# Kernel tuning notes

Hardware: AMD Instinct MI355X
Metric: run time of the kernel (lower is better)

The kernel has to match this reference:

```python
import jax, jax.numpy as jnp
import numpy as np

TANFOV = 1.0  # tan(FoV/2) for a 90-degree camera (both axes)
C0 = 0.28209479177387814
C1 = 0.4886025119029199
C2 = (1.0925484305920792, -1.0925484305920792, 0.31539156525252005, -1.0925484305920792, 0.5462742152960396)
C3 = (-0.5900435899266435, 2.890611442640554, -0.4570457994644658, 0.3731763325901154, -0.4570457994644658, 1.445305721320277, -0.5900435899266435)


def eval_sh3(sh, d):
    # sh: [N,16,3], d: [N,3] unit view dirs -> clamped RGB [N,3]
    x, y, z = d[:, 0:1], d[:, 1:2], d[:, 2:3]
    xx, yy, zz = x * x, y * y, z * z
    xy, yz, xz = x * y, y * z, x * z
    res = (C0 * sh[:, 0] - C1 * y * sh[:, 1] + C1 * z * sh[:, 2] - C1 * x * sh[:, 3]
           + C2[0] * xy * sh[:, 4] + C2[1] * yz * sh[:, 5] + C2[2] * (2 * zz - xx - yy) * sh[:, 6]
           + C2[3] * xz * sh[:, 7] + C2[4] * (xx - yy) * sh[:, 8]
           + C3[0] * y * (3 * xx - yy) * sh[:, 9] + C3[1] * xy * z * sh[:, 10]
           + C3[2] * y * (4 * zz - xx - yy) * sh[:, 11] + C3[3] * z * (2 * zz - 3 * xx - 3 * yy) * sh[:, 12]
           + C3[4] * x * (4 * zz - xx - yy) * sh[:, 13] + C3[5] * z * (xx - yy) * sh[:, 14]
           + C3[6] * x * (xx - 3 * yy) * sh[:, 15])
    return jnp.maximum(res + 0.5, 0.0)


def quat_to_rot(q):
    w, x, y, z = q[:, 0], q[:, 1], q[:, 2], q[:, 3]
    r0 = jnp.stack([1 - 2 * (y * y + z * z), 2 * (x * y - w * z), 2 * (x * z + w * y)], -1)
    r1 = jnp.stack([2 * (x * y + w * z), 1 - 2 * (x * x + z * z), 2 * (y * z - w * x)], -1)
    r2 = jnp.stack([2 * (x * z - w * y), 2 * (y * z + w * x), 1 - 2 * (x * x + y * y)], -1)
    return jnp.stack([r0, r1, r2], -2)  # [N,3,3]


def gaussian_render(xyz, scaling, rotation, opacity, features_dc, features_rest,
                    viewmatrix, projmatrix, campos, bg, H, W):
    N = xyz.shape[0]
    # --- activation wrappers (GaussianModel properties) ---
    scales = jnp.exp(scaling)                      # [N,3]
    op = jax.nn.sigmoid(opacity)[:, 0]             # [N]
    qn = rotation / jnp.maximum(jnp.linalg.norm(rotation, axis=-1, keepdims=True), 1e-12)
    shs = jnp.concatenate([features_dc, features_rest], axis=1)  # [N,16,3]
    # --- SH -> RGB ---
    dirs = xyz - campos[None, :]
    dirs = dirs / jnp.maximum(jnp.linalg.norm(dirs, axis=-1, keepdims=True), 1e-12)
    colors = eval_sh3(shs, dirs)                   # [N,3]
    # --- 3D covariance: Sigma = R S S^T R^T ---
    R = quat_to_rot(qn)
    M = R * scales[:, None, :]
    Sigma = M @ jnp.swapaxes(M, -1, -2)            # [N,3,3]
    # --- camera space (torch row-vector convention: p_view = p @ V[:3,:3] + V[3,:3]) ---
    t = xyz @ viewmatrix[:3, :3] + viewmatrix[3, :3]
    tz = t[:, 2]
    fx = W / (2.0 * TANFOV)
    fy = H / (2.0 * TANFOV)
    lim = 1.3 * TANFOV
    tz_safe = jnp.where(jnp.abs(tz) > 1e-6, tz, 1e-6)
    txz = jnp.clip(t[:, 0] / tz_safe, -lim, lim) * tz_safe
    tyz = jnp.clip(t[:, 1] / tz_safe, -lim, lim) * tz_safe
    zeros = jnp.zeros_like(tz)
    J = jnp.stack([jnp.stack([fx / tz_safe, zeros, -fx * txz / (tz_safe * tz_safe)], -1),
                   jnp.stack([zeros, fy / tz_safe, -fy * tyz / (tz_safe * tz_safe)], -1)], -2)  # [N,2,3]
    Wr = viewmatrix[:3, :3].T
    Tm = J @ Wr[None, :, :]                        # [N,2,3]
    cov2 = Tm @ Sigma @ jnp.swapaxes(Tm, -1, -2)   # [N,2,2]
    a = cov2[:, 0, 0] + 0.3
    b = cov2[:, 0, 1]
    c = cov2[:, 1, 1] + 0.3
    det = a * c - b * b
    valid = (tz > 0.2) & (det > 0)
    inv_det = 1.0 / jnp.where(det > 0, det, 1.0)
    conA, conB, conC = c * inv_det, -b * inv_det, a * inv_det
    # --- screen radius (3 sigma of max eigenvalue) ---
    mid = 0.5 * (a + c)
    lam = mid + jnp.sqrt(jnp.maximum(mid * mid - det, 0.1))
    radii = jnp.where(valid, jnp.ceil(3.0 * jnp.sqrt(lam)), 0.0)
    # --- project means with full_proj_transform ---
    p_hom = jnp.concatenate([xyz, jnp.ones((N, 1), xyz.dtype)], axis=1) @ projmatrix
    pw = 1.0 / (p_hom[:, 3] + 1e-7)
    mx = ((p_hom[:, 0] * pw + 1.0) * W - 1.0) * 0.5
    my = ((p_hom[:, 1] * pw + 1.0) * H - 1.0) * 0.5
    # --- per-pixel Gaussian evaluation ---
    ys, xs = jnp.meshgrid(jnp.arange(H, dtype=xyz.dtype), jnp.arange(W, dtype=xyz.dtype), indexing='ij')
    px = xs.reshape(-1)  # [HW]
    py = ys.reshape(-1)
    dx = px[:, None] - mx[None, :]                 # [HW,N]
    dy = py[:, None] - my[None, :]
    power = -0.5 * (conA[None, :] * dx * dx + conC[None, :] * dy * dy) - conB[None, :] * dx * dy
    alpha = jnp.minimum(0.99, op[None, :] * jnp.exp(jnp.minimum(power, 0.0)))
    skip = (power > 0) | (alpha < (1.0 / 255.0)) | (~valid)[None, :]
    alpha = jnp.where(skip, 0.0, alpha)
    # --- global depth sort + front-to-back alpha compositing ---
    order = jnp.argsort(tz)
    alpha_s = alpha[:, order]
    cols_s = colors[order]
    tz_s = tz[order]
    Tcum = jnp.cumprod(1.0 - alpha_s, axis=1)      # [HW,N]
    Texcl = jnp.concatenate([jnp.ones((H * W, 1), alpha_s.dtype), Tcum[:, :-1]], axis=1)
    wgt = alpha_s * Texcl                          # [HW,N]
    img = wgt @ cols_s + Tcum[:, -1:] * bg[None, :]
    color = img.reshape(H, W, 3).transpose(2, 0, 1)          # [3,H,W]
    depth = (wgt @ tz_s[:, None]).reshape(1, H, W)           # [1,H,W]
    amap = (1.0 - Tcum[:, -1]).reshape(1, H, W)              # [1,H,W]
    return color, depth, amap, radii


def setup_inputs() -> dict:
    key = jax.random.key(0)
    ks = jax.random.split(key, 6)
    N, H, W = 2048, 128, 128
    xyz = 0.7 * jax.random.normal(ks[0], (N, 3), jnp.float32)
    scaling = jnp.log(0.03) + 0.3 * jax.random.normal(ks[1], (N, 3), jnp.float32)
    rotation = jax.random.normal(ks[2], (N, 4), jnp.float32)
    opacity = jax.random.normal(ks[3], (N, 1), jnp.float32) - 1.0
    features_dc = 0.5 * jax.random.normal(ks[4], (N, 1, 3), jnp.float32)
    features_rest = 0.05 * jax.random.normal(ks[5], (N, 15, 3), jnp.float32)
    # camera at (0,0,-4) looking down +z; transposed (row-vector) matrices as in torch 3DGS
    view = np.eye(4, dtype=np.float32)
    view[3, 2] = 4.0
    znear, zfar = 0.01, 100.0
    P = np.zeros((4, 4), dtype=np.float32)
    P[0, 0] = 1.0 / TANFOV
    P[1, 1] = 1.0 / TANFOV
    P[2, 2] = zfar / (zfar - znear)
    P[3, 2] = -(zfar * znear) / (zfar - znear)
    P[2, 3] = 1.0
    full_proj = view @ P
    campos = jnp.array([0.0, 0.0, -4.0], jnp.float32)
    bg = jnp.zeros(3, jnp.float32)
    return {"xyz": xyz, "scaling": scaling, "rotation": rotation, "opacity": opacity,
            "features_dc": features_dc, "features_rest": features_rest,
            "viewmatrix": jnp.asarray(view), "projmatrix": jnp.asarray(full_proj),
            "campos": campos, "bg": bg, "image_height": H, "image_width": W}


def reference(xyz, scaling, rotation, opacity, features_dc, features_rest,
              viewmatrix, projmatrix, campos, bg, image_height, image_width):
    return gaussian_render(xyz, scaling, rotation, opacity, features_dc, features_rest,
                           viewmatrix, projmatrix, campos, bg, int(image_height), int(image_width))
```

## Files before the change

### kernel.cpp

```cpp
#include <hip/hip_runtime.h>
#include <math.h>

#define TANFOV 1.0f

#define REC   12
#define CHG   256
#define SEG_L 128

__global__ __launch_bounds__(256)
void pre_count_kernel(
    const float* __restrict__ xyz, const float* __restrict__ scaling,
    const float* __restrict__ rotation, const float* __restrict__ opacity,
    const float* __restrict__ fdc, const float* __restrict__ frest,
    const float* __restrict__ vm, const float* __restrict__ pm,
    const float* __restrict__ campos,
    const int* __restrict__ pH, const int* __restrict__ pW,
    float* __restrict__ pre, float4* __restrict__ bboxpre,
    int* __restrict__ rankpart, float* __restrict__ radii_out,
    int N, int NB, int NJ)
{
    __shared__ float s_fr[256 * 45];
    const int tid = threadIdx.x;
    const int bid = blockIdx.x;

    if (bid >= NB) {
        float* s_tz = s_fr;
        int t = bid - NB;
        int col = t / NJ, seg = t - col * NJ;
        int base = seg * SEG_L;
        float c2 = vm[2], c6 = vm[6], c10 = vm[10], c14 = vm[14];
        if (tid < SEG_L) {
            int j = base + tid;
            s_tz[tid] = (j < N)
                ? xyz[j*3+0]*c2 + xyz[j*3+1]*c6 + xyz[j*3+2]*c10 + c14
                : 3.4e38f;
        }
        __syncthreads();

        int i = col * 256 + tid;
        if (i < N) {
            float key = xyz[i*3+0]*c2 + xyz[i*3+1]*c6 + xyz[i*3+2]*c10 + c14;
            int cnt = 0;
            #pragma unroll 8
            for (int j = 0; j < SEG_L; j += 4) {
                float4 v = *reinterpret_cast<float4*>(&s_tz[j]);
                cnt += (v.x < key) || (v.x == key && (base + j)     < i);
                cnt += (v.y < key) || (v.y == key && (base + j + 1) < i);
                cnt += (v.z < key) || (v.z == key && (base + j + 2) < i);
                cnt += (v.w < key) || (v.w == key && (base + j + 3) < i);
            }
            rankpart[seg * N + i] = cnt;
        }
        return;
    }

    int i0 = bid * 256;
    int cnt = N - i0; if (cnt > 256) cnt = 256;
    for (int t = tid; t < cnt * 45; t += 256)
        s_fr[t] = frest[(size_t)i0 * 45 + t];
    __syncthreads();

    int i = i0 + tid;
    if (i >= N) return;
    float H = (float)*pH, W = (float)*pW;

    float px_ = xyz[i*3+0], py_ = xyz[i*3+1], pz_ = xyz[i*3+2];
    float s0 = expf(scaling[i*3+0]), s1 = expf(scaling[i*3+1]), s2 = expf(scaling[i*3+2]);
    float op = 1.f / (1.f + expf(-opacity[i]));

    float qw = rotation[i*4+0], qx = rotation[i*4+1], qy = rotation[i*4+2], qz = rotation[i*4+3];
    float qn = fmaxf(sqrtf(qw*qw + qx*qx + qy*qy + qz*qz), 1e-12f);
    qw /= qn; qx /= qn; qy /= qn; qz /= qn;

    float R00 = 1.f - 2.f*(qy*qy + qz*qz), R01 = 2.f*(qx*qy - qw*qz), R02 = 2.f*(qx*qz + qw*qy);
    float R10 = 2.f*(qx*qy + qw*qz), R11 = 1.f - 2.f*(qx*qx + qz*qz), R12 = 2.f*(qy*qz - qw*qx);
    float R20 = 2.f*(qx*qz - qw*qy), R21 = 2.f*(qy*qz + qw*qx), R22 = 1.f - 2.f*(qx*qx + qy*qy);

    float M00 = R00*s0, M01 = R01*s1, M02 = R02*s2;
    float M10 = R10*s0, M11 = R11*s1, M12 = R12*s2;
    float M20 = R20*s0, M21 = R21*s1, M22 = R22*s2;

    float S00 = M00*M00 + M01*M01 + M02*M02;
    float S01 = M00*M10 + M01*M11 + M02*M12;
    float S02 = M00*M20 + M01*M21 + M02*M22;
    float S11 = M10*M10 + M11*M11 + M12*M12;
    float S12 = M10*M20 + M11*M21 + M12*M22;
    float S22 = M20*M20 + M21*M21 + M22*M22;

    float t0 = px_*vm[0] + py_*vm[4] + pz_*vm[8]  + vm[12];
    float t1 = px_*vm[1] + py_*vm[5] + pz_*vm[9]  + vm[13];
    float tz = px_*vm[2] + py_*vm[6] + pz_*vm[10] + vm[14];

    float fx = W / (2.f * TANFOV), fy = H / (2.f * TANFOV);
    float lim = 1.3f * TANFOV;
    float tzs = (fabsf(tz) > 1e-6f) ? tz : 1e-6f;
    float txz = fminf(fmaxf(t0 / tzs, -lim), lim) * tzs;
    float tyz = fminf(fmaxf(t1 / tzs, -lim), lim) * tzs;
    float J00 = fx / tzs, J02 = -fx * txz / (tzs * tzs);
    float J11 = fy / tzs, J12 = -fy * tyz / (tzs * tzs);

    float T00 = J00*vm[0] + J02*vm[2];
    float T01 = J00*vm[4] + J02*vm[6];
    float T02 = J00*vm[8] + J02*vm[10];
    float T10 = J11*vm[1] + J12*vm[2];
    float T11 = J11*vm[5] + J12*vm[6];
    float T12 = J11*vm[9] + J12*vm[10];

    float u0 = S00*T00 + S01*T01 + S02*T02;
    float u1 = S01*T00 + S11*T01 + S12*T02;
    float u2 = S02*T00 + S12*T01 + S22*T02;
    float v0 = S00*T10 + S01*T11 + S02*T12;
    float v1 = S01*T10 + S11*T11 + S12*T12;
    float v2 = S02*T10 + S12*T11 + S22*T12;
    float a  = T00*u0 + T01*u1 + T02*u2 + 0.3f;
    float b  = T10*u0 + T11*u1 + T12*u2;
    float c  = T10*v0 + T11*v1 + T12*v2 + 0.3f;

    float det = a*c - b*b;
    bool valid = (tz > 0.2f) && (det > 0.f);
    float inv_det = 1.f / ((det > 0.f) ? det : 1.f);
    float conA = c * inv_det, conB = -b * inv_det, conC = a * inv_det;
    float mid = 0.5f * (a + c);
    float lam = mid + sqrtf(fmaxf(mid*mid - det, 0.1f));
    radii_out[i] = valid ? ceilf(3.f * sqrtf(lam)) : 0.f;

    float h0 = px_*pm[0] + py_*pm[4] + pz_*pm[8]  + pm[12];
    float h1 = px_*pm[1] + py_*pm[5] + pz_*pm[9]  + pm[13];
    float h3 = px_*pm[3] + py_*pm[7] + pz_*pm[11] + pm[15];
    float pw = 1.f / (h3 + 1e-7f);
    float mx = ((h0*pw + 1.f) * W - 1.f) * 0.5f;
    float my = ((h1*pw + 1.f) * H - 1.f) * 0.5f;

    float ddx = px_ - campos[0], ddy = py_ - campos[1], ddz = pz_ - campos[2];
    float dn = fmaxf(sqrtf(ddx*ddx + ddy*ddy + ddz*ddz), 1e-12f);
    float x = ddx/dn, y = ddy/dn, z = ddz/dn;
    float xx = x*x, yy = y*y, zz = z*z, xy = x*y, yz = y*z, xz = x*z;

    float basis[16];
    basis[0]  = 0.28209479177387814f;
    basis[1]  = -0.4886025119029199f * y;
    basis[2]  =  0.4886025119029199f * z;
    basis[3]  = -0.4886025119029199f * x;
    basis[4]  =  1.0925484305920792f * xy;
    basis[5]  = -1.0925484305920792f * yz;
    basis[6]  =  0.31539156525252005f * (2.f*zz - xx - yy);
    basis[7]  = -1.0925484305920792f * xz;
    basis[8]  =  0.5462742152960396f * (xx - yy);
    basis[9]  = -0.5900435899266435f * y * (3.f*xx - yy);
    basis[10] =  2.890611442640554f  * xy * z;
    basis[11] = -0.4570457994644658f * y * (4.f*zz - xx - yy);
    basis[12] =  0.3731763325901154f * z * (2.f*zz - 3.f*xx - 3.f*yy);
    basis[13] = -0.4570457994644658f * x * (4.f*zz - xx - yy);
    basis[14] =  1.445305721320277f  * z * (xx - yy);
    basis[15] = -0.5900435899266435f * x * (xx - 3.f*yy);

    const float* fr = &s_fr[tid * 45];
    float col[3];
    #pragma unroll
    for (int ch = 0; ch < 3; ++ch) {
        float r = basis[0] * fdc[i*3 + ch];
        #pragma unroll
        for (int j = 1; j < 16; ++j)
            r += basis[j] * fr[(j-1)*3 + ch];
        col[ch] = fmaxf(r + 0.5f, 0.f);
    }

    float opv = valid ? op : 0.f;
    float4* rec = (float4*)(pre + (size_t)i * REC);
    rec[0] = make_float4(tz, -0.5f*conA, -conB, -0.5f*conC);
    rec[1] = make_float4(mx, my, opv, 0.f);
    rec[2] = make_float4(col[0], col[1], col[2], 0.f);

    float4 bb;
    if (opv > 1.f/255.f) {
        float Rr = 1.01f * sqrtf(2.f * logf(255.f * opv) * lam) + 1.f;
        bb = make_float4(mx - Rr, mx + Rr, my - Rr, my + Rr);
    } else {
        bb = make_float4(1e30f, -1e30f, 1e30f, -1e30f);
    }
    bboxpre[i] = bb;
}

__global__ void scatter_kernel(const int* __restrict__ rankpart,
                               int* __restrict__ perm, int N, int NJ)
{
    int i = blockIdx.x * blockDim.x + threadIdx.x;
    if (i >= N) return;
    int rank = 0;
    for (int s = 0; s < NJ; ++s) rank += rankpart[s * N + i];
    perm[rank] = i;
}

__global__ void blend1_kernel(const float4* __restrict__ grec,
                              const float4* __restrict__ bbox,
                              const int* __restrict__ perm,
                              const int* __restrict__ pW,
                              float* __restrict__ part,
                              int N, int HW, int G)
{
    __shared__ int    s_cnt[4];
    __shared__ int    s_idx[CHG];
    __shared__ float4 s_rec[3 * CHG];

    int tid = threadIdx.x;
    int W = *pW;
    int tilesX = (W + 15) >> 4;
    int tileX = blockIdx.x % tilesX;
    int tileY = blockIdx.x / tilesX;
    int px = (tileX << 4) + (tid & 15);
    int py = (tileY << 4) + (tid >> 4);
    int pix = py * W + px;
    float fpx = (float)px, fpy = (float)py;
    float ftx0 = (float)(tileX << 4), ftx1 = ftx0 + 15.f;
    float fty0 = (float)(tileY << 4), fty1 = fty0 + 15.f;

    int chunk = blockIdx.y;
    int g0 = chunk * CHG;
    int S = G * HW;

    int g = g0 + tid;
    bool hit = false;
    int orig = 0;
    if (g < N) {
        orig = perm[g];
        float4 bb = bbox[orig];
        hit = (bb.x <= ftx1) && (bb.y >= ftx0) &&
              (bb.z <= fty1) && (bb.w >= fty0);
    }
    unsigned long long m = __ballot(hit);
    int lane = tid & 63, wv = tid >> 6;
    int pos = __popcll(m & ((1ull << lane) - 1ull));
    if (lane == 0) s_cnt[wv] = __popcll(m);
    __syncthreads();
    int total = s_cnt[0] + s_cnt[1] + s_cnt[2] + s_cnt[3];
    int off = 0;
    for (int w = 0; w < wv; ++w) off += s_cnt[w];
    if (hit) s_idx[off + pos] = orig;
    __syncthreads();

    for (int k = tid; k < 3 * total; k += CHG) {
        int s = k / 3, e = k - 3 * s;
        s_rec[k] = grec[3 * s_idx[s] + e];
    }
    __syncthreads();

    float T = 1.f, c0 = 0.f, c1 = 0.f, c2 = 0.f, d = 0.f;
    for (int s = 0; s < total; ++s) {
        float4 pA = s_rec[3*s+0];
        float4 pB = s_rec[3*s+1];
        float4 pC = s_rec[3*s+2];
        float dx = fpx - pB.x, dy = fpy - pB.y;
        float power = pA.y*dx*dx + pA.w*dy*dy + pA.z*dx*dy;
        float alpha = fminf(0.99f, pB.z * __expf(fminf(power, 0.f)));
        bool keep = (power <= 0.f) && (alpha >= 1.f/255.f);
        float aeff = keep ? alpha : 0.f;
        float w = aeff * T;
        c0 = fmaf(w, pC.x, c0);
        c1 = fmaf(w, pC.y, c1);
        c2 = fmaf(w, pC.z, c2);
        d  = fmaf(w, pA.x, d);
        T  = T - aeff * T;
    }
    if (pix < HW) {
        int o = chunk * HW + pix;
        part[0*S+o] = c0; part[1*S+o] = c1; part[2*S+o] = c2;
        part[3*S+o] = d;  part[4*S+o] = T;
    }
}

__global__ void blend2_kernel(const float* __restrict__ part,
                              const float* __restrict__ bg,
                              float* __restrict__ out, int HW, int G)
{
    int pix = blockIdx.x * blockDim.x + threadIdx.x;
    if (pix >= HW) return;
    int S = G * HW;
    float T = 1.f, c0 = 0.f, c1 = 0.f, c2 = 0.f, d = 0.f;
    for (int k = 0; k < G; ++k) {
        int o = k * HW + pix;
        c0 += T * part[0*S+o];
        c1 += T * part[1*S+o];
        c2 += T * part[2*S+o];
        d  += T * part[3*S+o];
        T  *= part[4*S+o];
    }
    out[0*HW+pix] = c0 + T*bg[0];
    out[1*HW+pix] = c1 + T*bg[1];
    out[2*HW+pix] = c2 + T*bg[2];
    out[3*HW+pix] = d;
    out[4*HW+pix] = 1.f - T;
}

extern "C" void kernel_launch(void* const* d_in, const int* in_sizes, int n_in,
                              void* d_out, int out_size, void* d_ws, size_t ws_size,
                              hipStream_t stream) {
    const float* xyz      = (const float*)d_in[0];
    const float* scaling  = (const float*)d_in[1];
    const float* rotation = (const float*)d_in[2];
    const float* opacity  = (const float*)d_in[3];
    const float* fdc      = (const float*)d_in[4];
    const float* frest    = (const float*)d_in[5];
    const float* vm       = (const float*)d_in[6];
    const float* pm       = (const float*)d_in[7];
    const float* campos   = (const float*)d_in[8];
    const float* bg       = (const float*)d_in[9];
    const int*   pH       = (const int*)d_in[10];
    const int*   pW       = (const int*)d_in[11];

    int N  = in_sizes[0] / 3;
    int HW = (out_size - N) / 5;
    int G  = (N + CHG - 1) / CHG;
    int NJ = (N + SEG_L - 1) / SEG_L;
    int NB = (N + 255) / 256;
    int NT = (HW + 255) / 256;

    float*  ws       = (float*)d_ws;
    float*  pre      = ws;
    float4* bboxpre  = (float4*)(pre + (size_t)REC * N);
    int*    rankpart = (int*)(bboxpre + N);
    int*    perm     = rankpart + (size_t)NJ * N;
    float*  part     = (float*)(perm + N);

    float* out   = (float*)d_out;
    float* radii = out + (size_t)5 * HW;

    pre_count_kernel<<<NB + NB * NJ, 256, 0, stream>>>(
        xyz, scaling, rotation, opacity, fdc, frest, vm, pm, campos, pH, pW,
        pre, bboxpre, rankpart, radii, N, NB, NJ);
    scatter_kernel<<<NB, 256, 0, stream>>>(rankpart, perm, N, NJ);
    dim3 bgrid(NT, G);
    blend1_kernel<<<bgrid, CHG, 0, stream>>>(
        (const float4*)pre, bboxpre, perm, pW, part, N, HW, G);
    blend2_kernel<<<NT, 256, 0, stream>>>(part, bg, out, HW, G);
}
```

Before: 32.71 us.

## Fuse scatter, chunked blend, and composite into a single per-tile render kernel

```diff
diff --git a/kernel.cpp b/kernel.cpp
--- a/kernel.cpp
+++ b/kernel.cpp
@@ -181,28 +181,29 @@
     bboxpre[i] = bb;
 }
 
-__global__ void scatter_kernel(const int* __restrict__ rankpart,
-                               int* __restrict__ perm, int N, int NJ)
+__global__ __launch_bounds__(256)
+void render_tiles_kernel(const float4* __restrict__ grec,
+                         const float4* __restrict__ bbox,
+                         const int* __restrict__ rankpart,
+                         const int* __restrict__ pW,
+                         const float* __restrict__ bg,
+                         float* __restrict__ out,
+                         int N, int HW, int G, int NJ)
 {
-    int i = blockIdx.x * blockDim.x + threadIdx.x;
-    if (i >= N) return;
-    int rank = 0;
-    for (int s = 0; s < NJ; ++s) rank += rankpart[s * N + i];
-    perm[rank] = i;
-}
-
-__global__ void blend1_kernel(const float4* __restrict__ grec,
-                              const float4* __restrict__ bbox,
-                              const int* __restrict__ perm,
-                              const int* __restrict__ pW,
-                              float* __restrict__ part,
-                              int N, int HW, int G)
-{
+    extern __shared__ int s_perm[];
     __shared__ int    s_cnt[4];
     __shared__ int    s_idx[CHG];
     __shared__ float4 s_rec[3 * CHG];
 
-    int tid = threadIdx.x;
+    const int tid = threadIdx.x;
+
+    for (int i = tid; i < N; i += CHG) {
+        int rank = 0;
+        #pragma unroll 4
+        for (int s = 0; s < NJ; ++s) rank += rankpart[s * N + i];
+        s_perm[rank] = i;
+    }
+
     int W = *pW;
     int tilesX = (W + 15) >> 4;
     int tileX = blockIdx.x % tilesX;
@@ -213,82 +214,62 @@
     float fpx = (float)px, fpy = (float)py;
     float ftx0 = (float)(tileX << 4), ftx1 = ftx0 + 15.f;
     float fty0 = (float)(tileY << 4), fty1 = fty0 + 15.f;
-
-    int chunk = blockIdx.y;
-    int g0 = chunk * CHG;
-    int S = G * HW;
-
-    int g = g0 + tid;
-    bool hit = false;
-    int orig = 0;
-    if (g < N) {
-        orig = perm[g];
-        float4 bb = bbox[orig];
-        hit = (bb.x <= ftx1) && (bb.y >= ftx0) &&
-              (bb.z <= fty1) && (bb.w >= fty0);
-    }
-    unsigned long long m = __ballot(hit);
-    int lane = tid & 63, wv = tid >> 6;
-    int pos = __popcll(m & ((1ull << lane) - 1ull));
-    if (lane == 0) s_cnt[wv] = __popcll(m);
     __syncthreads();
-    int total = s_cnt[0] + s_cnt[1] + s_cnt[2] + s_cnt[3];
-    int off = 0;
-    for (int w = 0; w < wv; ++w) off += s_cnt[w];
-    if (hit) s_idx[off + pos] = orig;
-    __syncthreads();
-
-    for (int k = tid; k < 3 * total; k += CHG) {
-        int s = k / 3, e = k - 3 * s;
-        s_rec[k] = grec[3 * s_idx[s] + e];
-    }
-    __syncthreads();
 
     float T = 1.f, c0 = 0.f, c1 = 0.f, c2 = 0.f, d = 0.f;
-    for (int s = 0; s < total; ++s) {
-        float4 pA = s_rec[3*s+0];
-        float4 pB = s_rec[3*s+1];
-        float4 pC = s_rec[3*s+2];
-        float dx = fpx - pB.x, dy = fpy - pB.y;
-        float power = pA.y*dx*dx + pA.w*dy*dy + pA.z*dx*dy;
-        float alpha = fminf(0.99f, pB.z * __expf(fminf(power, 0.f)));
-        bool keep = (power <= 0.f) && (alpha >= 1.f/255.f);
-        float aeff = keep ? alpha : 0.f;
-        float w = aeff * T;
-        c0 = fmaf(w, pC.x, c0);
-        c1 = fmaf(w, pC.y, c1);
-        c2 = fmaf(w, pC.z, c2);
-        d  = fmaf(w, pA.x, d);
-        T  = T - aeff * T;
-    }
+
+    for (int chunk = 0; chunk < G; ++chunk) {
+        int g = chunk * CHG + tid;
+        bool hit = false;
+        int orig = 0;
+        if (g < N) {
+            orig = s_perm[g];
+            float4 bb = bbox[orig];
+            hit = (bb.x <= ftx1) && (bb.y >= ftx0) &&
+                  (bb.z <= fty1) && (bb.w >= fty0);
+        }
+        unsigned long long m = __ballot(hit);
+        int lane = tid & 63, wv = tid >> 6;
+        int pos = __popcll(m & ((1ull << lane) - 1ull));
+        if (lane == 0) s_cnt[wv] = __popcll(m);
+        __syncthreads();
+        int total = s_cnt[0] + s_cnt[1] + s_cnt[2] + s_cnt[3];
+        int off = 0;
+        for (int w = 0; w < wv; ++w) off += s_cnt[w];
+        if (hit) s_idx[off + pos] = orig;
+        __syncthreads();
+
+        for (int k = tid; k < 3 * total; k += CHG) {
+            int s = k / 3, e = k - 3 * s;
+            s_rec[k] = grec[3 * s_idx[s] + e];
+        }
+        __syncthreads();
+
+        for (int s = 0; s < total; ++s) {
+            float4 pA = s_rec[3*s+0];
+            float4 pB = s_rec[3*s+1];
+            float4 pC = s_rec[3*s+2];
+            float dx = fpx - pB.x, dy = fpy - pB.y;
+            float power = pA.y*dx*dx + pA.w*dy*dy + pA.z*dx*dy;
+            float alpha = fminf(0.99f, pB.z * __expf(fminf(power, 0.f)));
+            bool keep = (power <= 0.f) && (alpha >= 1.f/255.f);
+            float aeff = keep ? alpha : 0.f;
+            float w = aeff * T;
+            c0 = fmaf(w, pC.x, c0);
+            c1 = fmaf(w, pC.y, c1);
+            c2 = fmaf(w, pC.z, c2);
+            d  = fmaf(w, pA.x, d);
+            T  = T - aeff * T;
+        }
+    }
+
     if (pix < HW) {
-        int o = chunk * HW + pix;
-        part[0*S+o] = c0; part[1*S+o] = c1; part[2*S+o] = c2;
-        part[3*S+o] = d;  part[4*S+o] = T;
-    }
-}
-
-__global__ void blend2_kernel(const float* __restrict__ part,
-                              const float* __restrict__ bg,
-                              float* __restrict__ out, int HW, int G)
-{
-    int pix = blockIdx.x * blockDim.x + threadIdx.x;
-    if (pix >= HW) return;
-    int S = G * HW;
-    float T = 1.f, c0 = 0.f, c1 = 0.f, c2 = 0.f, d = 0.f;
-    for (int k = 0; k < G; ++k) {
-        int o = k * HW + pix;
-        c0 += T * part[0*S+o];
-        c1 += T * part[1*S+o];
-        c2 += T * part[2*S+o];
-        d  += T * part[3*S+o];
-        T  *= part[4*S+o];
-    }
-    out[0*HW+pix] = c0 + T*bg[0];
-    out[1*HW+pix] = c1 + T*bg[1];
-    out[2*HW+pix] = c2 + T*bg[2];
-    out[3*HW+pix] = d;
-    out[4*HW+pix] = 1.f - T;
+        out[0*HW+pix] = c0 + T*bg[0];
+        out[1*HW+pix] = c1 + T*bg[1];
+        out[2*HW+pix] = c2 + T*bg[2];
+        out[3*HW+pix] = d;
+        out[4*HW+pix] = 1.f - T;
+    }
 }
 
 extern "C" void kernel_launch(void* const* d_in, const int* in_sizes, int n_in,
@@ -318,8 +299,6 @@
     float*  pre      = ws;
     float4* bboxpre  = (float4*)(pre + (size_t)REC * N);
     int*    rankpart = (int*)(bboxpre + N);
-    int*    perm     = rankpart + (size_t)NJ * N;
-    float*  part     = (float*)(perm + N);
 
     float* out   = (float*)d_out;
     float* radii = out + (size_t)5 * HW;
@@ -327,9 +306,6 @@
     pre_count_kernel<<<NB + NB * NJ, 256, 0, stream>>>(
         xyz, scaling, rotation, opacity, fdc, frest, vm, pm, campos, pH, pW,
         pre, bboxpre, rankpart, radii, N, NB, NJ);
-    scatter_kernel<<<NB, 256, 0, stream>>>(rankpart, perm, N, NJ);
-    dim3 bgrid(NT, G);
-    blend1_kernel<<<bgrid, CHG, 0, stream>>>(
-        (const float4*)pre, bboxpre, perm, pW, part, N, HW, G);
-    blend2_kernel<<<NT, 256, 0, stream>>>(part, bg, out, HW, G);
+    render_tiles_kernel<<<NT, CHG, (size_t)N * sizeof(int), stream>>>(
+        (const float4*)pre, bboxpre, rankpart, pW, bg, out, N, HW, G, NJ);
 }
```

Result: slower. 76.32 us (+133.3%).

## Fuse rank scatter into blend kernel and widen rank-count segments

Applied to the files above, without the earlier changes.

```diff
diff --git a/kernel.cpp b/kernel.cpp
--- a/kernel.cpp
+++ b/kernel.cpp
@@ -5,7 +5,7 @@
 
 #define REC   12
 #define CHG   256
-#define SEG_L 128
+#define SEG_L 256
 
 __global__ __launch_bounds__(256)
 void pre_count_kernel(
@@ -181,28 +181,43 @@
     bboxpre[i] = bb;
 }
 
-__global__ void scatter_kernel(const int* __restrict__ rankpart,
-                               int* __restrict__ perm, int N, int NJ)
+__global__ __launch_bounds__(256)
+void blend1_kernel(const float4* __restrict__ grec,
+                   const float4* __restrict__ bbox,
+                   const int* __restrict__ rankpart,
+                   const int* __restrict__ pW,
+                   float* __restrict__ part,
+                   int N, int HW, int G, int NJ)
 {
-    int i = blockIdx.x * blockDim.x + threadIdx.x;
-    if (i >= N) return;
-    int rank = 0;
-    for (int s = 0; s < NJ; ++s) rank += rankpart[s * N + i];
-    perm[rank] = i;
-}
-
-__global__ void blend1_kernel(const float4* __restrict__ grec,
-                              const float4* __restrict__ bbox,
-                              const int* __restrict__ perm,
-                              const int* __restrict__ pW,
-                              float* __restrict__ part,
-                              int N, int HW, int G)
-{
+    __shared__ int    s_perm[CHG];
     __shared__ int    s_cnt[4];
     __shared__ int    s_idx[CHG];
     __shared__ float4 s_rec[3 * CHG];
 
-    int tid = threadIdx.x;
+    const int tid = threadIdx.x;
+    const int chunk = blockIdx.y;
+    const int g0 = chunk * CHG;
+
+    int rk[8];
+    #pragma unroll
+    for (int b = 0; b < 8; ++b) rk[b] = 0;
+    for (int s = 0; s < NJ; ++s) {
+        const int* rp = rankpart + s * N;
+        #pragma unroll
+        for (int b = 0; b < 8; ++b) {
+            int i = (b << 8) + tid;
+            rk[b] += (i < N) ? rp[i] : 0;
+        }
+    }
+    #pragma unroll
+    for (int b = 0; b < 8; ++b) {
+        int i = (b << 8) + tid;
+        if (i < N) {
+            unsigned r = (unsigned)(rk[b] - g0);
+            if (r < (unsigned)CHG) s_perm[r] = i;
+        }
+    }
+
     int W = *pW;
     int tilesX = (W + 15) >> 4;
     int tileX = blockIdx.x % tilesX;
@@ -213,16 +228,13 @@
     float fpx = (float)px, fpy = (float)py;
     float ftx0 = (float)(tileX << 4), ftx1 = ftx0 + 15.f;
     float fty0 = (float)(tileY << 4), fty1 = fty0 + 15.f;
-
-    int chunk = blockIdx.y;
-    int g0 = chunk * CHG;
-    int S = G * HW;
+    __syncthreads();
 
     int g = g0 + tid;
     bool hit = false;
     int orig = 0;
     if (g < N) {
-        orig = perm[g];
+        orig = s_perm[tid];
         float4 bb = bbox[orig];
         hit = (bb.x <= ftx1) && (bb.y >= ftx0) &&
               (bb.z <= fty1) && (bb.w >= fty0);
@@ -263,6 +275,7 @@
     }
     if (pix < HW) {
         int o = chunk * HW + pix;
+        int S = G * HW;
         part[0*S+o] = c0; part[1*S+o] = c1; part[2*S+o] = c2;
         part[3*S+o] = d;  part[4*S+o] = T;
     }
@@ -318,8 +331,7 @@
     float*  pre      = ws;
     float4* bboxpre  = (float4*)(pre + (size_t)REC * N);
     int*    rankpart = (int*)(bboxpre + N);
-    int*    perm     = rankpart + (size_t)NJ * N;
-    float*  part     = (float*)(perm + N);
+    float*  part     = (float*)(rankpart + (size_t)NJ * N);
 
     float* out   = (float*)d_out;
     float* radii = out + (size_t)5 * HW;
@@ -327,9 +339,8 @@
     pre_count_kernel<<<NB + NB * NJ, 256, 0, stream>>>(
         xyz, scaling, rotation, opacity, fdc, frest, vm, pm, campos, pH, pW,
         pre, bboxpre, rankpart, radii, N, NB, NJ);
-    scatter_kernel<<<NB, 256, 0, stream>>>(rankpart, perm, N, NJ);
     dim3 bgrid(NT, G);
     blend1_kernel<<<bgrid, CHG, 0, stream>>>(
-        (const float4*)pre, bboxpre, perm, pW, part, N, HW, G);
+        (const float4*)pre, bboxpre, rankpart, pW, part, N, HW, G, NJ);
     blend2_kernel<<<NT, 256, 0, stream>>>(part, bg, out, HW, G);
 }
```

Result: slower. 34.40 us (+5.2%).
